# Kernel tuning notes

Hardware: AMD Instinct MI355X
Metric: run time of the kernel (lower is better)

Reference implementation:

```python
import jax, jax.numpy as jnp
import numpy as np

GROUPS = 32
N_HEADS = 16
EPS = 1e-5


def setup_inputs() -> dict:
    key = jax.random.key(0)
    ks = jax.random.split(key, 5)
    b, c, t = 4, 1024, 1024
    return {
        "x": jax.random.normal(ks[0], (b, c, t), dtype=jnp.float32),
        "gn_weight": jnp.ones((c,), dtype=jnp.float32),
        "gn_bias": jnp.zeros((c,), dtype=jnp.float32),
        "qkv_w": jax.random.normal(ks[1], (3 * c, c), dtype=jnp.float32) * (c ** -0.5),
        "qkv_b": jax.random.normal(ks[2], (3 * c,), dtype=jnp.float32) * 0.02,
        "proj_w": jax.random.normal(ks[3], (c, c), dtype=jnp.float32) * (c ** -0.5),
        "proj_b": jax.random.normal(ks[4], (c,), dtype=jnp.float32) * 0.02,
    }


def _group_norm(x, weight, bias):
    # x: [b, c, t]; GroupNorm32 computes stats in float32 (already fp32 here)
    b, c, t = x.shape
    xg = x.reshape(b, GROUPS, c // GROUPS, t)
    mean = xg.mean(axis=(2, 3), keepdims=True)
    var = xg.var(axis=(2, 3), keepdims=True)
    xn = ((xg - mean) * jax.lax.rsqrt(var + EPS)).reshape(b, c, t)
    return xn * weight[None, :, None] + bias[None, :, None]


def reference(x, gn_weight, gn_bias, qkv_w, qkv_b, proj_w, proj_b):
    b, c, t = x.shape
    xn = _group_norm(x, gn_weight, gn_bias)
    # 1x1 Conv1d == channel matmul: [3c, c] x [b, c, t] -> [b, 3c, t]
    qkv = jnp.einsum('oc,bct->bot', qkv_w, xn) + qkv_b[None, :, None]
    ch = c // N_HEADS
    # legacy per-head interleaved layout: reshape to [b*H, 3*ch, t], split
    qkv = qkv.reshape(b * N_HEADS, 3 * ch, t)
    q, k, v = qkv[:, :ch], qkv[:, ch:2 * ch], qkv[:, 2 * ch:]
    scale = ch ** -0.25  # 1/sqrt(sqrt(ch)), applied to both q and k
    weight = jnp.einsum('bct,bcs->bts', q * scale, k * scale)  # [b*H, t, t]
    weight = jax.nn.softmax(weight.astype(jnp.float32), axis=-1).astype(weight.dtype)
    a = jnp.einsum('bts,bcs->bct', weight, v).reshape(b, c, t)
    h = jnp.einsum('oc,bct->bot', proj_w, a) + proj_b[None, :, None]
    return x + h
```

## Files before the change

### kernel.cpp

```cpp
#include <hip/hip_runtime.h>
#include <hip/hip_bf16.h>

typedef __bf16 bf16;
typedef __bf16 bf16x2 __attribute__((ext_vector_type(2)));
typedef __bf16 bf16x4 __attribute__((ext_vector_type(4)));
typedef __bf16 bf16x8 __attribute__((ext_vector_type(8)));
typedef float  f32x4  __attribute__((ext_vector_type(4)));

static __device__ __forceinline__ f32x4 mfma16(bf16x8 a, bf16x8 b, f32x4 c) {
  return __builtin_amdgcn_mfma_f32_16x16x32_bf16(a, b, c, 0, 0, 0);
}

static __device__ __forceinline__ void gload_lds16(const bf16* g, bf16* l) {
  __builtin_amdgcn_global_load_lds(
      (const __attribute__((address_space(1))) void*)g,
      (__attribute__((address_space(3))) void*)l, 16, 0, 0);
}

#define VMCNT0() asm volatile("s_waitcnt vmcnt(0)" ::: "memory")
#define VMCNT2() asm volatile("s_waitcnt vmcnt(2)" ::: "memory")
#define VMCNT4() asm volatile("s_waitcnt vmcnt(4)" ::: "memory")
#define BARRIER()                                        \
  do {                                                   \
    asm volatile("" ::: "memory");                       \
    __builtin_amdgcn_s_barrier();                        \
    asm volatile("" ::: "memory");                       \
  } while (0)

__global__ __launch_bounds__(512) void pre_kernel(const float* __restrict__ x,
                                                  const float* __restrict__ gw,
                                                  const float* __restrict__ gb,
                                                  bf16* __restrict__ xnT,
                                                  const float* __restrict__ qkv_w,
                                                  bf16* __restrict__ wq,
                                                  const float* __restrict__ proj_w,
                                                  bf16* __restrict__ wp) {
  int blk = blockIdx.x;
  int tid = threadIdx.x;
  if (blk >= 512) {
    int i = (blk - 512) * 512 + tid;
    const int na4 = 3072 * 1024 / 4;
    const float* src; bf16* dst;
    if (i < na4) { src = qkv_w; dst = wq; }
    else         { src = proj_w; dst = wp; i -= na4; }
    float4 v = ((const float4*)src)[i];
    bf16x4 o = { (bf16)v.x, (bf16)v.y, (bf16)v.z, (bf16)v.w };
    *(bf16x4*)(dst + 4ll * i) = o;
    return;
  }
  int id = blk;
  int b = id >> 7, g = (id >> 2) & 31, qtr = id & 3;
  const float* xb = x + ((size_t)b * 1024 + g * 32) * 1024;
  float s = 0.f, sq = 0.f;
  const float4* x4 = (const float4*)xb;
  for (int i = tid; i < 8192; i += 512) {
    float4 v = x4[i];
    s  += v.x + v.y + v.z + v.w;
    sq += v.x * v.x + v.y * v.y + v.z * v.z + v.w * v.w;
  }
#pragma unroll
  for (int off = 32; off; off >>= 1) { s += __shfl_down(s, off); sq += __shfl_down(sq, off); }
  __shared__ float red[16];
  int wv = tid >> 6;
  if ((tid & 63) == 0) { red[wv] = s; red[8 + wv] = sq; }
  __syncthreads();
  s = 0.f; sq = 0.f;
#pragma unroll
  for (int i = 0; i < 8; ++i) { s += red[i]; sq += red[8 + i]; }
  float mean = s * (1.f / 32768.f);
  float var  = sq * (1.f / 32768.f) - mean * mean;
  float rstd = rsqrtf(var + 1e-5f);

  __shared__ bf16 tile[64][36];
  int c = tid >> 4, q = tid & 15;
  int r = tid >> 3, q2 = tid & 7;
  float wc = gw[g * 32 + c] * rstd;
  float fb = gb[g * 32 + c] - mean * wc;
  for (int t0 = qtr * 256; t0 < qtr * 256 + 256; t0 += 64) {
    float4 v = *(const float4*)(xb + (size_t)c * 1024 + t0 + q * 4);
    tile[q * 4 + 0][c] = (bf16)(v.x * wc + fb);
    tile[q * 4 + 1][c] = (bf16)(v.y * wc + fb);
    tile[q * 4 + 2][c] = (bf16)(v.z * wc + fb);
    tile[q * 4 + 3][c] = (bf16)(v.w * wc + fb);
    __syncthreads();
    *(bf16x4*)&xnT[((size_t)b * 1024 + t0 + r) * 1024 + g * 32 + q2 * 4] =
        *(bf16x4*)&tile[r][q2 * 4];
    __syncthreads();
  }
}

__global__ __launch_bounds__(512, 1) void qkv_kernel(
    const bf16* __restrict__ A, const bf16* __restrict__ Bw,
    const float* __restrict__ bias,
    bf16* __restrict__ qkT, bf16* __restrict__ vC) {
  extern __shared__ __align__(16) bf16 smem[];

  int tid = threadIdx.x, wid = tid >> 6, lane = tid & 63;
  int l15 = lane & 15, l4 = lane >> 4;
  int wr = wid >> 2, wc = wid & 3;
  int rsw = (l15 & 7) << 4;

  int sid = (blockIdx.x & 7) * 32 + (blockIdx.x >> 3);
  int bx = sid & 15, by = (sid >> 4) & 3, z = sid >> 6;
  int m0 = by * 256, n0 = bx * 192;
  const bf16* Ab = A + (size_t)z * 1024 * 1024 + (size_t)m0 * 1024;
  const bf16* Bb = Bw + (size_t)n0 * 1024;

  int srow = tid >> 3;
  int csw  = (tid & 7) ^ (srow & 7);
  auto stageA = [&](int d, int kt) {
    bf16* dst = smem + d * 16384;
    const bf16* src = Ab + kt * 64 + csw * 8;
#pragma unroll
    for (int hh = 0; hh < 2; ++hh)
#pragma unroll
      for (int L = 0; L < 2; ++L)
        gload_lds16(src + (size_t)(hh * 128 + L * 64 + srow) * 1024,
                    dst + hh * 8192 + (L * 512 + wid * 64) * 8);
  };
  auto stageB = [&](int d, int kt) {
    bf16* dst = smem + 49152 + d * 12288;
    const bf16* src = Bb + kt * 64 + csw * 8;
#pragma unroll
    for (int L = 0; L < 3; ++L)
      gload_lds16(src + (size_t)(L * 64 + srow) * 1024, dst + (L * 512 + wid * 64) * 8);
  };

  f32x4 acc[8][3] = {};

  auto compute = [&](int ta, int tb) {
    const char* Ab8 = (const char*)smem + ta * 32768 + wr * 16384;
    const char* Bb8 = (const char*)smem + 98304 + tb * 24576;
    bf16x8 bfr[3][2], af[4][2];
#pragma unroll
    for (int ni = 0; ni < 3; ++ni) {
      int rb = (wc * 48 + ni * 16 + l15) * 128;
#pragma unroll
      for (int kk = 0; kk < 2; ++kk)
        bfr[ni][kk] = *(const bf16x8*)(Bb8 + rb + ((kk * 64 + l4 * 16) ^ rsw));
    }
#pragma unroll
    for (int mi = 0; mi < 4; ++mi) {
      int rb = (mi * 16 + l15) * 128;
#pragma unroll
      for (int kk = 0; kk < 2; ++kk)
        af[mi][kk] = *(const bf16x8*)(Ab8 + rb + ((kk * 64 + l4 * 16) ^ rsw));
    }
#pragma unroll
    for (int mi = 0; mi < 4; ++mi)
#pragma unroll
      for (int ni = 0; ni < 3; ++ni)
#pragma unroll
        for (int kk = 0; kk < 2; ++kk)
          acc[mi][ni] = mfma16(af[mi][kk], bfr[ni][kk], acc[mi][ni]);
#pragma unroll
    for (int mi = 0; mi < 4; ++mi) {
      int rb = ((4 + mi) * 16 + l15) * 128;
#pragma unroll
      for (int kk = 0; kk < 2; ++kk)
        af[mi][kk] = *(const bf16x8*)(Ab8 + rb + ((kk * 64 + l4 * 16) ^ rsw));
    }
#pragma unroll
    for (int mi = 0; mi < 4; ++mi)
#pragma unroll
      for (int ni = 0; ni < 3; ++ni)
#pragma unroll
        for (int kk = 0; kk < 2; ++kk)
          acc[4 + mi][ni] = mfma16(af[mi][kk], bfr[ni][kk], acc[4 + mi][ni]);
  };

  stageA(0, 0); stageB(0, 0); stageA(1, 1);
  VMCNT4();
  BARRIER();

  for (int t = 0; t < 14; ++t) {
    stageB((t + 1) & 1, t + 1);
    stageA((t + 2) % 3, t + 2);
    compute(t % 3, t & 1);
    VMCNT4();
    BARRIER();
  }
  stageB(1, 15);
  compute(2, 0);
  VMCNT0();
  BARRIER();
  compute(0, 1);

  const float scale = 0.35355339059327373f;
  int h = bx;
#pragma unroll
  for (int ni = 0; ni < 3; ++ni) {
    int oin = wc * 48 + ni * 16;
    float bv = bias[n0 + oin + l15];
#pragma unroll
    for (int mi = 0; mi < 8; ++mi) {
      int tb = m0 + wr * 128 + mi * 16 + l4 * 4;
      f32x4 v = acc[mi][ni];
      if (oin < 128) {
#pragma unroll
        for (int i = 0; i < 4; ++i)
          qkT[((size_t)z * 1024 + tb + i) * 2048 + h * 128 + oin + l15] =
              (bf16)((v[i] + bv) * scale);
      } else {
        bf16x4 st = { (bf16)(v[0] + bv), (bf16)(v[1] + bv),
                      (bf16)(v[2] + bv), (bf16)(v[3] + bv) };
        *(bf16x4*)&vC[(((size_t)z * 16 + h) * 64 + (oin - 128 + l15)) * 1024 + tb] = st;
      }
    }
  }
}

__global__ __launch_bounds__(512, 1) void proj_kernel(
    const bf16* __restrict__ A, const bf16* __restrict__ Bw,
    const float* __restrict__ bias,
    const float* __restrict__ xres, float* __restrict__ out) {
  extern __shared__ __align__(16) bf16 smem[];

  int tid = threadIdx.x, wid = tid >> 6, lane = tid & 63;
  int l15 = lane & 15, l4 = lane >> 4;
  int wr = wid >> 2, wc = wid & 3;
  int rsw = (l15 & 7) << 4;

  int sid = (blockIdx.x & 7) * 32 + (blockIdx.x >> 3);
  int bx = sid & 7, by = (sid >> 3) & 7, z = sid >> 6;
  int m0 = by * 128, n0 = bx * 128;
  const bf16* Ab = A + (size_t)z * 1024 * 1024 + (size_t)m0 * 1024;
  const bf16* Bb = Bw + (size_t)n0 * 1024;

  int srow = tid >> 3;
  int csw  = (tid & 7) ^ (srow & 7);
  auto stageA = [&](int d, int kt) {
    bf16* dst = smem + d * 8192;
    const bf16* src = Ab + kt * 64 + csw * 8;
#pragma unroll
    for (int L = 0; L < 2; ++L)
      gload_lds16(src + (size_t)(L * 64 + srow) * 1024, dst + (L * 512 + wid * 64) * 8);
  };
  auto stageB = [&](int d, int kt) {
    bf16* dst = smem + 24576 + d * 8192;
    const bf16* src = Bb + kt * 64 + csw * 8;
#pragma unroll
    for (int L = 0; L < 2; ++L)
      gload_lds16(src + (size_t)(L * 64 + srow) * 1024, dst + (L * 512 + wid * 64) * 8);
  };

  f32x4 acc[4][2] = {};

  auto compute = [&](int ta, int tb) {
    const char* Ab8 = (const char*)smem + ta * 16384 + wr * 8192;
    const char* Bb8 = (const char*)smem + 49152 + tb * 16384;
    bf16x8 bfr[2][2], af[4][2];
#pragma unroll
    for (int ni = 0; ni < 2; ++ni) {
      int rb = (wc * 32 + ni * 16 + l15) * 128;
#pragma unroll
      for (int kk = 0; kk < 2; ++kk)
        bfr[ni][kk] = *(const bf16x8*)(Bb8 + rb + ((kk * 64 + l4 * 16) ^ rsw));
    }
#pragma unroll
    for (int mi = 0; mi < 4; ++mi) {
      int rb = (mi * 16 + l15) * 128;
#pragma unroll
      for (int kk = 0; kk < 2; ++kk)
        af[mi][kk] = *(const bf16x8*)(Ab8 + rb + ((kk * 64 + l4 * 16) ^ rsw));
    }
#pragma unroll
    for (int mi = 0; mi < 4; ++mi)
#pragma unroll
      for (int ni = 0; ni < 2; ++ni)
#pragma unroll
        for (int kk = 0; kk < 2; ++kk)
          acc[mi][ni] = mfma16(af[mi][kk], bfr[ni][kk], acc[mi][ni]);
  };

  stageA(0, 0); stageB(0, 0); stageA(1, 1);
  VMCNT2();
  BARRIER();

  for (int t = 0; t < 14; ++t) {
    stageB((t + 1) & 1, t + 1);
    stageA((t + 2) % 3, t + 2);
    compute(t % 3, t & 1);
    VMCNT2();
    BARRIER();
  }
  stageB(1, 15);
  compute(2, 0);
  VMCNT0();
  BARRIER();
  compute(0, 1);

#pragma unroll
  for (int ni = 0; ni < 2; ++ni) {
    int o = n0 + wc * 32 + ni * 16 + l15;
    float bv = bias[o];
#pragma unroll
    for (int mi = 0; mi < 4; ++mi) {
      int tb = m0 + wr * 64 + mi * 16 + l4 * 4;
      size_t base = ((size_t)z * 1024 + o) * 1024 + tb;
      float4 xr = *(const float4*)(xres + base);
      f32x4 v = acc[mi][ni];
      float4 ov = { xr.x + v[0] + bv, xr.y + v[1] + bv,
                    xr.z + v[2] + bv, xr.w + v[3] + bv };
      *(float4*)(out + base) = ov;
    }
  }
}

__global__ __launch_bounds__(512, 4) void attn_kernel(const bf16* __restrict__ qkT,
                                                      const bf16* __restrict__ vC,
                                                      bf16* __restrict__ aT) {
  __shared__ __align__(16) bf16 Kt[2][64 * 64];
  __shared__ __align__(16) bf16 Vt[2][64 * 64];
  __shared__ __align__(16) bf16 Pt[8][16 * 64];

  int id = blockIdx.x;
  int sid = (id & 7) * 64 + (id >> 3);
  int head = sid >> 3, tblk = sid & 7;
  int b = head >> 4, h = head & 15;
  int t0 = tblk * 128;
  int tid = threadIdx.x, wid = tid >> 6, lane = tid & 63;
  int l15 = lane & 15, l4 = lane >> 4;
  int trow = t0 + wid * 16;

  const bf16* kbase = qkT + (size_t)b * 1024 * 2048 + h * 128 + 64;
  const bf16* vbase = vC + (size_t)(b * 16 + h) * 64 * 1024;
  char* Pw = (char*)Pt[wid];
  int rsw = (l15 & 7) << 4;
  char* PwRow = Pw + l15 * 128;

  const bf16* qrow = qkT + ((size_t)b * 1024 + trow + l15) * 2048 + h * 128;
  bf16x8 qf[2];
#pragma unroll
  for (int kb = 0; kb < 2; ++kb) qf[kb] = *(const bf16x8*)(qrow + kb * 32 + l4 * 8);

  int rl = lane >> 3;
  int scol = (((lane & 7) * 16) ^ (rl << 4)) >> 1;
  int r8 = wid * 8 + rl;
  auto stage = [&](int buf, int st) {
    int s0 = st * 64;
    gload_lds16(kbase + (size_t)(s0 + r8) * 2048 + scol, &Kt[buf][wid * 512]);
    gload_lds16(vbase + (size_t)r8 * 1024 + s0 + scol, &Vt[buf][wid * 512]);
  };

  float m_run = -1e30f, l_run = 0.f;
  f32x4 oacc[4] = {};

  stage(0, 0);
  __syncthreads();

  for (int st = 0; st < 16; ++st) {
    int cur = st & 1;
    if (st < 15) stage(cur ^ 1, st + 1);

    const char* Kb = (const char*)Kt[cur];
    f32x4 sf[4];
#pragma unroll
    for (int nf = 0; nf < 4; ++nf) sf[nf] = (f32x4){0.f, 0.f, 0.f, 0.f};
    __builtin_amdgcn_s_setprio(1);
#pragma unroll
    for (int nf = 0; nf < 4; ++nf) {
      int rr = nf * 16 + l15;
#pragma unroll
      for (int kb = 0; kb < 2; ++kb) {
        bf16x8 kf = *(const bf16x8*)(Kb + rr * 128 + ((kb * 64 + l4 * 16) ^ rsw));
        sf[nf] = mfma16(kf, qf[kb], sf[nf]);
      }
    }
    __builtin_amdgcn_s_setprio(0);

    float mb;
    {
      float a0 = fmaxf(fmaxf(sf[0][0], sf[0][1]), fmaxf(sf[0][2], sf[0][3]));
      float a1 = fmaxf(fmaxf(sf[1][0], sf[1][1]), fmaxf(sf[1][2], sf[1][3]));
      float a2 = fmaxf(fmaxf(sf[2][0], sf[2][1]), fmaxf(sf[2][2], sf[2][3]));
      float a3 = fmaxf(fmaxf(sf[3][0], sf[3][1]), fmaxf(sf[3][2], sf[3][3]));
      mb = fmaxf(fmaxf(a0, a1), fmaxf(a2, a3));
    }
    mb = fmaxf(mb, __shfl_xor(mb, 16));
    mb = fmaxf(mb, __shfl_xor(mb, 32));
    if (!__all(mb - m_run <= 8.f)) {
      float mn = fmaxf(m_run, mb);
      float corr = __expf(m_run - mn);
      m_run = mn;
      l_run *= corr;
#pragma unroll
      for (int cf = 0; cf < 4; ++cf)
#pragma unroll
        for (int i = 0; i < 4; ++i) oacc[cf][i] *= corr;
    }
    float sb = 0.f;
#pragma unroll
    for (int nf = 0; nf < 4; ++nf) {
      float p0 = __expf(sf[nf][0] - m_run), p1 = __expf(sf[nf][1] - m_run);
      float p2 = __expf(sf[nf][2] - m_run), p3 = __expf(sf[nf][3] - m_run);
      sb += (p0 + p1) + (p2 + p3);
      int off = nf * 32 + l4 * 8;
      *(bf16x4*)(PwRow + (off ^ rsw)) = (bf16x4){ (bf16)p0, (bf16)p1, (bf16)p2, (bf16)p3 };
    }
    sb += __shfl_xor(sb, 16);
    sb += __shfl_xor(sb, 32);
    l_run += sb;

    const char* Vb = (const char*)Vt[cur];
    __builtin_amdgcn_s_setprio(1);
#pragma unroll
    for (int kb = 0; kb < 2; ++kb) {
      bf16x8 pf = *(const bf16x8*)(Pw + l15 * 128 + ((kb * 64 + l4 * 16) ^ rsw));
#pragma unroll
      for (int cf = 0; cf < 4; ++cf) {
        int rr = cf * 16 + l15;
        bf16x8 vf = *(const bf16x8*)(Vb + rr * 128 + ((kb * 64 + l4 * 16) ^ rsw));
        oacc[cf] = mfma16(vf, pf, oacc[cf]);
      }
    }
    __builtin_amdgcn_s_setprio(0);
    __syncthreads();
  }

  float rdiv = 1.f / l_run;
  int t = trow + l15;
#pragma unroll
  for (int cf = 0; cf < 4; ++cf) {
    bf16x4 ov = { (bf16)(oacc[cf][0] * rdiv), (bf16)(oacc[cf][1] * rdiv),
                  (bf16)(oacc[cf][2] * rdiv), (bf16)(oacc[cf][3] * rdiv) };
    *(bf16x4*)&aT[((size_t)b * 1024 + t) * 1024 + h * 64 + cf * 16 + l4 * 4] = ov;
  }
}

extern "C" void kernel_launch(void* const* d_in, const int* in_sizes, int n_in,
                              void* d_out, int out_size, void* d_ws, size_t ws_size,
                              hipStream_t stream) {
  const float* x      = (const float*)d_in[0];
  const float* gw     = (const float*)d_in[1];
  const float* gb     = (const float*)d_in[2];
  const float* qkv_w  = (const float*)d_in[3];
  const float* qkv_b  = (const float*)d_in[4];
  const float* proj_w = (const float*)d_in[5];
  const float* proj_b = (const float*)d_in[6];
  float* out = (float*)d_out;

  char* ws = (char*)d_ws;
  bf16* wq_bf = (bf16*)(ws);
  bf16* wp_bf = (bf16*)(ws + 6ll  * 1024 * 1024);
  bf16* xnT   = (bf16*)(ws + 8ll  * 1024 * 1024);
  bf16* qkT   = (bf16*)(ws + 16ll * 1024 * 1024);
  bf16* vC    = (bf16*)(ws + 32ll * 1024 * 1024);
  bf16* aT    = (bf16*)(ws + 40ll * 1024 * 1024);

  hipFuncSetAttribute(reinterpret_cast<const void*>(qkv_kernel),
                      hipFuncAttributeMaxDynamicSharedMemorySize, 147456);
  hipFuncSetAttribute(reinterpret_cast<const void*>(proj_kernel),
                      hipFuncAttributeMaxDynamicSharedMemorySize, 81920);

  pre_kernel<<<dim3(2560), dim3(512), 0, stream>>>(x, gw, gb, xnT, qkv_w, wq_bf, proj_w, wp_bf);
  qkv_kernel<<<dim3(256), dim3(512), 147456, stream>>>(xnT, wq_bf, qkv_b, qkT, vC);
  attn_kernel<<<dim3(512), dim3(512), 0, stream>>>(qkT, vC, aT);
  proj_kernel<<<dim3(256), dim3(512), 81920, stream>>>(aT, wp_bf, proj_b, x, out);
}
```

Before: 96.33 us.

## Switch attention to 32x32 MFMA with register-resident P via permlane swap

The attention kernel moves from 16x16x32 to 32x32x16 bf16 MFMA tiles, with each wave now covering 32 query rows and the block shrunk to 4 waves. The softmax probabilities are packed with v_cvt_pk_bf16_f32 and rearranged across half-waves with v_permlane32_swap, so they feed the PV MFMA straight from registers instead of going through an LDS scratch buffer. This removes the P store/load round trip and a shuffle stage, and gives larger MFMA tiles with more reuse per operand. The cost is more accumulator registers per lane and half as many waves per block, which could lower occupancy or latency hiding.

Result: no change. 96.52 us (+0.2%).

```diff
diff --git a/kernel.cpp b/kernel.cpp
--- a/kernel.cpp
+++ b/kernel.cpp
@@ -6,15 +6,28 @@
 typedef __bf16 bf16x4 __attribute__((ext_vector_type(4)));
 typedef __bf16 bf16x8 __attribute__((ext_vector_type(8)));
 typedef float  f32x4  __attribute__((ext_vector_type(4)));
+typedef float  f32x16 __attribute__((ext_vector_type(16)));
 
 static __device__ __forceinline__ f32x4 mfma16(bf16x8 a, bf16x8 b, f32x4 c) {
   return __builtin_amdgcn_mfma_f32_16x16x32_bf16(a, b, c, 0, 0, 0);
+}
+static __device__ __forceinline__ f32x16 mfma32(bf16x8 a, bf16x8 b, f32x16 c) {
+  return __builtin_amdgcn_mfma_f32_32x32x16_bf16(a, b, c, 0, 0, 0);
 }
 
 static __device__ __forceinline__ void gload_lds16(const bf16* g, bf16* l) {
   __builtin_amdgcn_global_load_lds(
       (const __attribute__((address_space(1))) void*)g,
       (__attribute__((address_space(3))) void*)l, 16, 0, 0);
+}
+
+static __device__ __forceinline__ int cvtpk(float lo, float hi) {
+  int w;
+  asm("v_cvt_pk_bf16_f32 %0, %1, %2" : "=v"(w) : "v"(lo), "v"(hi));
+  return w;
+}
+static __device__ __forceinline__ void plswap(int& x, int& y) {
+  asm("v_permlane32_swap_b32 %0, %1" : "+v"(x), "+v"(y));
 }
 
 #define VMCNT0() asm volatile("s_waitcnt vmcnt(0)" ::: "memory")
@@ -307,12 +320,11 @@
   }
 }
 
-__global__ __launch_bounds__(512, 4) void attn_kernel(const bf16* __restrict__ qkT,
+__global__ __launch_bounds__(256, 3) void attn_kernel(const bf16* __restrict__ qkT,
                                                       const bf16* __restrict__ vC,
                                                       bf16* __restrict__ aT) {
   __shared__ __align__(16) bf16 Kt[2][64 * 64];
   __shared__ __align__(16) bf16 Vt[2][64 * 64];
-  __shared__ __align__(16) bf16 Pt[8][16 * 64];
 
   int id = blockIdx.x;
   int sid = (id & 7) * 64 + (id >> 3);
@@ -320,31 +332,33 @@
   int b = head >> 4, h = head & 15;
   int t0 = tblk * 128;
   int tid = threadIdx.x, wid = tid >> 6, lane = tid & 63;
-  int l15 = lane & 15, l4 = lane >> 4;
-  int trow = t0 + wid * 16;
+  int l31 = lane & 31, hi = lane >> 5;
+  int trow = t0 + wid * 32;
 
   const bf16* kbase = qkT + (size_t)b * 1024 * 2048 + h * 128 + 64;
   const bf16* vbase = vC + (size_t)(b * 16 + h) * 64 * 1024;
-  char* Pw = (char*)Pt[wid];
-  int rsw = (l15 & 7) << 4;
-  char* PwRow = Pw + l15 * 128;
-
-  const bf16* qrow = qkT + ((size_t)b * 1024 + trow + l15) * 2048 + h * 128;
-  bf16x8 qf[2];
-#pragma unroll
-  for (int kb = 0; kb < 2; ++kb) qf[kb] = *(const bf16x8*)(qrow + kb * 32 + l4 * 8);
+  int rsw = (lane & 7) << 4;
+
+  const bf16* qrow = qkT + ((size_t)b * 1024 + trow + l31) * 2048 + h * 128;
+  bf16x8 qf[4];
+#pragma unroll
+  for (int kb = 0; kb < 4; ++kb) qf[kb] = *(const bf16x8*)(qrow + kb * 16 + hi * 8);
 
   int rl = lane >> 3;
   int scol = (((lane & 7) * 16) ^ (rl << 4)) >> 1;
-  int r8 = wid * 8 + rl;
   auto stage = [&](int buf, int st) {
     int s0 = st * 64;
-    gload_lds16(kbase + (size_t)(s0 + r8) * 2048 + scol, &Kt[buf][wid * 512]);
-    gload_lds16(vbase + (size_t)r8 * 1024 + s0 + scol, &Vt[buf][wid * 512]);
+#pragma unroll
+    for (int j = 0; j < 2; ++j) {
+      int g8 = wid * 2 + j;
+      int r = g8 * 8 + rl;
+      gload_lds16(kbase + (size_t)(s0 + r) * 2048 + scol, &Kt[buf][g8 * 512]);
+      gload_lds16(vbase + (size_t)r * 1024 + s0 + scol, &Vt[buf][g8 * 512]);
+    }
   };
 
   float m_run = -1e30f, l_run = 0.f;
-  f32x4 oacc[4] = {};
+  f32x16 oacc[2] = {};
 
   stage(0, 0);
   __syncthreads();
@@ -354,30 +368,28 @@
     if (st < 15) stage(cur ^ 1, st + 1);
 
     const char* Kb = (const char*)Kt[cur];
-    f32x4 sf[4];
-#pragma unroll
-    for (int nf = 0; nf < 4; ++nf) sf[nf] = (f32x4){0.f, 0.f, 0.f, 0.f};
+    f32x16 sf[2] = {};
     __builtin_amdgcn_s_setprio(1);
 #pragma unroll
-    for (int nf = 0; nf < 4; ++nf) {
-      int rr = nf * 16 + l15;
-#pragma unroll
-      for (int kb = 0; kb < 2; ++kb) {
-        bf16x8 kf = *(const bf16x8*)(Kb + rr * 128 + ((kb * 64 + l4 * 16) ^ rsw));
-        sf[nf] = mfma16(kf, qf[kb], sf[nf]);
+    for (int sb = 0; sb < 2; ++sb) {
+      int rowb = (sb * 32 + l31) * 128;
+#pragma unroll
+      for (int kb = 0; kb < 4; ++kb) {
+        bf16x8 kf = *(const bf16x8*)(Kb + rowb + ((kb * 32 + hi * 16) ^ rsw));
+        sf[sb] = mfma32(kf, qf[kb], sf[sb]);
       }
     }
     __builtin_amdgcn_s_setprio(0);
 
     float mb;
     {
-      float a0 = fmaxf(fmaxf(sf[0][0], sf[0][1]), fmaxf(sf[0][2], sf[0][3]));
-      float a1 = fmaxf(fmaxf(sf[1][0], sf[1][1]), fmaxf(sf[1][2], sf[1][3]));
-      float a2 = fmaxf(fmaxf(sf[2][0], sf[2][1]), fmaxf(sf[2][2], sf[2][3]));
-      float a3 = fmaxf(fmaxf(sf[3][0], sf[3][1]), fmaxf(sf[3][2], sf[3][3]));
-      mb = fmaxf(fmaxf(a0, a1), fmaxf(a2, a3));
-    }
-    mb = fmaxf(mb, __shfl_xor(mb, 16));
+      float m0v = fmaxf(sf[0][0], sf[0][1]);
+#pragma unroll
+      for (int r = 2; r < 16; ++r) m0v = fmaxf(m0v, sf[0][r]);
+#pragma unroll
+      for (int r = 0; r < 16; ++r) m0v = fmaxf(m0v, sf[1][r]);
+      mb = m0v;
+    }
     mb = fmaxf(mb, __shfl_xor(mb, 32));
     if (!__all(mb - m_run <= 8.f)) {
       float mn = fmaxf(m_run, mb);
@@ -385,33 +397,43 @@
       m_run = mn;
       l_run *= corr;
 #pragma unroll
-      for (int cf = 0; cf < 4; ++cf)
-#pragma unroll
-        for (int i = 0; i < 4; ++i) oacc[cf][i] *= corr;
-    }
-    float sb = 0.f;
-#pragma unroll
-    for (int nf = 0; nf < 4; ++nf) {
-      float p0 = __expf(sf[nf][0] - m_run), p1 = __expf(sf[nf][1] - m_run);
-      float p2 = __expf(sf[nf][2] - m_run), p3 = __expf(sf[nf][3] - m_run);
-      sb += (p0 + p1) + (p2 + p3);
-      int off = nf * 32 + l4 * 8;
-      *(bf16x4*)(PwRow + (off ^ rsw)) = (bf16x4){ (bf16)p0, (bf16)p1, (bf16)p2, (bf16)p3 };
-    }
-    sb += __shfl_xor(sb, 16);
-    sb += __shfl_xor(sb, 32);
-    l_run += sb;
+      for (int cb = 0; cb < 2; ++cb)
+#pragma unroll
+        for (int r = 0; r < 16; ++r) oacc[cb][r] *= corr;
+    }
+
+    float sbsum = 0.f;
+    bf16x8 pf[4];
+#pragma unroll
+    for (int sb = 0; sb < 2; ++sb) {
+      float p[16];
+#pragma unroll
+      for (int r = 0; r < 16; ++r) {
+        p[r] = __expf(sf[sb][r] - m_run);
+        sbsum += p[r];
+      }
+      int w0 = cvtpk(p[0], p[1]),   w1 = cvtpk(p[2], p[3]);
+      int w2 = cvtpk(p[4], p[5]),   w3 = cvtpk(p[6], p[7]);
+      int w4 = cvtpk(p[8], p[9]),   w5 = cvtpk(p[10], p[11]);
+      int w6 = cvtpk(p[12], p[13]), w7 = cvtpk(p[14], p[15]);
+      plswap(w0, w2); plswap(w1, w3);
+      plswap(w4, w6); plswap(w5, w7);
+      int4 f0 = { w0, w1, w2, w3 };
+      int4 f1 = { w4, w5, w6, w7 };
+      pf[sb * 2 + 0] = *(bf16x8*)&f0;
+      pf[sb * 2 + 1] = *(bf16x8*)&f1;
+    }
+    sbsum += __shfl_xor(sbsum, 32);
+    l_run += sbsum;
 
     const char* Vb = (const char*)Vt[cur];
     __builtin_amdgcn_s_setprio(1);
 #pragma unroll
-    for (int kb = 0; kb < 2; ++kb) {
-      bf16x8 pf = *(const bf16x8*)(Pw + l15 * 128 + ((kb * 64 + l4 * 16) ^ rsw));
-#pragma unroll
-      for (int cf = 0; cf < 4; ++cf) {
-        int rr = cf * 16 + l15;
-        bf16x8 vf = *(const bf16x8*)(Vb + rr * 128 + ((kb * 64 + l4 * 16) ^ rsw));
-        oacc[cf] = mfma16(vf, pf, oacc[cf]);
+    for (int ks = 0; ks < 4; ++ks) {
+#pragma unroll
+      for (int cb = 0; cb < 2; ++cb) {
+        bf16x8 vf = *(const bf16x8*)(Vb + (cb * 32 + l31) * 128 + ((ks * 32 + hi * 16) ^ rsw));
+        oacc[cb] = mfma32(vf, pf[ks], oacc[cb]);
       }
     }
     __builtin_amdgcn_s_setprio(0);
@@ -419,12 +441,16 @@
   }
 
   float rdiv = 1.f / l_run;
-  int t = trow + l15;
-#pragma unroll
-  for (int cf = 0; cf < 4; ++cf) {
-    bf16x4 ov = { (bf16)(oacc[cf][0] * rdiv), (bf16)(oacc[cf][1] * rdiv),
-                  (bf16)(oacc[cf][2] * rdiv), (bf16)(oacc[cf][3] * rdiv) };
-    *(bf16x4*)&aT[((size_t)b * 1024 + t) * 1024 + h * 64 + cf * 16 + l4 * 4] = ov;
+  int t = trow + l31;
+#pragma unroll
+  for (int cb = 0; cb < 2; ++cb) {
+#pragma unroll
+    for (int q = 0; q < 4; ++q) {
+      bf16x4 ov = { (bf16)(oacc[cb][q * 4 + 0] * rdiv), (bf16)(oacc[cb][q * 4 + 1] * rdiv),
+                    (bf16)(oacc[cb][q * 4 + 2] * rdiv), (bf16)(oacc[cb][q * 4 + 3] * rdiv) };
+      int c0 = h * 64 + cb * 32 + hi * 4 + q * 8;
+      *(bf16x4*)&aT[((size_t)b * 1024 + t) * 1024 + c0] = ov;
+    }
   }
 }
 
@@ -455,6 +481,6 @@
 
   pre_kernel<<<dim3(2560), dim3(512), 0, stream>>>(x, gw, gb, xnT, qkv_w, wq_bf, proj_w, wp_bf);
   qkv_kernel<<<dim3(256), dim3(512), 147456, stream>>>(xnT, wq_bf, qkv_b, qkT, vC);
-  attn_kernel<<<dim3(512), dim3(512), 0, stream>>>(qkT, vC, aT);
+  attn_kernel<<<dim3(512), dim3(256), 0, stream>>>(qkT, vC, aT);
   proj_kernel<<<dim3(256), dim3(512), 81920, stream>>>(aT, wp_bf, proj_b, x, out);
 }
```
